# Kernel tuning notes

Measured on AMD Instinct MI355X. Metric: run time of the kernel, lower is better.

Reference implementation:

```python
import jax, jax.numpy as jnp
import numpy as np

B, N, D, H = 1, 4096, 768, 12
HD = D // H
SCALE = HD ** -0.5

def setup_inputs() -> dict:
    key = jax.random.key(0)
    k1, k2, k3 = jax.random.split(key, 3)
    x = jax.random.normal(k1, (B, N, D), dtype=jnp.float32)
    W_qkv = jax.random.normal(k2, (D, 3 * D), dtype=jnp.float32) * (D ** -0.5)
    W_out = jax.random.normal(k3, (D, D), dtype=jnp.float32) * (D ** -0.5)
    b_out = jnp.zeros((D,), dtype=jnp.float32)
    return {"x": x, "W_qkv": W_qkv, "W_out": W_out, "b_out": b_out}

def reference(x, W_qkv, W_out, b_out):
    # qkv projection: (B,N,3D)
    qkv = x @ W_qkv
    q, k, v = jnp.split(qkv, 3, axis=-1)
    # (B,N,D) -> (B,H,N,hd)
    def heads(t):
        return t.reshape(B, N, H, HD).transpose(0, 2, 1, 3)
    q, k, v = heads(q), heads(k), heads(v)
    scores = jnp.einsum('bhnd,bhmd->bhnm', q, k) * SCALE  # (B,H,N,N)
    attn = jax.nn.softmax(scores, axis=-1)
    out = jnp.einsum('bhnm,bhmd->bhnd', attn, v)
    out = out.transpose(0, 2, 1, 3).reshape(B, N, D)
    return out @ W_out + b_out
```

## Files before the change

kernel.cpp:

```cpp
#include <hip/hip_runtime.h>
#include <hip/hip_bf16.h>
#include <math.h>

typedef __attribute__((ext_vector_type(8))) short bf16x8;
typedef __attribute__((ext_vector_type(4))) short bf16x4;
typedef __attribute__((ext_vector_type(4))) float floatx4;
typedef __attribute__((ext_vector_type(4))) unsigned int uint4v;

constexpr int kN  = 4096;
constexpr int kD  = 768;
constexpr int kH  = 12;
constexpr int kHD = 64;
constexpr int k3D = 2304;
constexpr float kQScale = 0.18033688011112042f;

static __device__ __forceinline__ short f2b(float f) {
    __hip_bfloat16 h = __float2bfloat16(f);
    return *reinterpret_cast<short*>(&h);
}

static __device__ __forceinline__ float fast_exp2(float x) {
#if __has_builtin(__builtin_amdgcn_exp2f)
    return __builtin_amdgcn_exp2f(x);
#else
    return exp2f(x);
#endif
}

static __device__ __forceinline__ unsigned cvt_pk_bf16(float lo, float hi) {
    unsigned r;
    asm("v_cvt_pk_bf16_f32 %0, %1, %2" : "=v"(r) : "v"(lo), "v"(hi));
    return r;
}
static __device__ __forceinline__ void permlane32_swap(unsigned &a, unsigned &b) {
    asm("v_permlane32_swap_b32 %0, %1" : "+v"(a), "+v"(b));
}
static __device__ __forceinline__ void permlane16_swap(unsigned &a, unsigned &b) {
    asm("v_permlane16_swap_b32 %0, %1" : "+v"(a), "+v"(b));
}

static __device__ __forceinline__ void async_copy16(const void* g, void* l) {
    __builtin_amdgcn_global_load_lds(
        (const __attribute__((address_space(1))) void*)g,
        (__attribute__((address_space(3))) void*)l, 16, 0, 0);
}

constexpr int kBlkX  = 1536;
constexpr int kBlkWq = 72 * 24;
constexpr int kBlkWo = 24 * 24;

__global__ __launch_bounds__(256)
void prep(const float* __restrict__ x, const float* __restrict__ Wq,
          const float* __restrict__ Wo, short* __restrict__ Xb,
          short* __restrict__ WqT, short* __restrict__ WoT)
{
    const int bid = blockIdx.x;
    const int tid = threadIdx.x;
    if (bid < kBlkX) {
        const int i = bid * 256 + tid;
        const float4* s = reinterpret_cast<const float4*>(x + (size_t)i * 8);
        float4 a = s[0], b = s[1];
        bf16x8 v;
        v[0] = f2b(a.x); v[1] = f2b(a.y); v[2] = f2b(a.z); v[3] = f2b(a.w);
        v[4] = f2b(b.x); v[5] = f2b(b.y); v[6] = f2b(b.z); v[7] = f2b(b.w);
        *reinterpret_cast<bf16x8*>(Xb + (size_t)i * 8) = v;
        return;
    }
    const float* src; short* dst; int R, C, bx, by;
    if (bid < kBlkX + kBlkWq) {
        const int local = bid - kBlkX;
        src = Wq; dst = WqT; R = kD; C = k3D; bx = local % 72; by = local / 72;
    } else {
        const int local = bid - kBlkX - kBlkWq;
        src = Wo; dst = WoT; R = kD; C = kD; bx = local % 24; by = local / 24;
    }
    __shared__ float t[32][33];
    const int c0 = bx * 32, r0 = by * 32;
    const int tx = tid & 31, ty = tid >> 5;
    #pragma unroll
    for (int i = ty; i < 32; i += 8)
        t[i][tx] = src[(size_t)(r0 + i) * C + c0 + tx];
    __syncthreads();
    #pragma unroll
    for (int i = ty; i < 32; i += 8)
        dst[(size_t)(c0 + i) * R + r0 + tx] = f2b(t[tx][i]);
}

template<int MODE>
__device__ __forceinline__
void gemm_core(const short* __restrict__ A, const short* __restrict__ BT,
               const float* __restrict__ bias, float* __restrict__ Cout,
               short* __restrict__ Qh, short* __restrict__ Kh, short* __restrict__ Vt,
               int N, int K)
{
    const int bm   = blockIdx.x * 128;
    const int bn   = blockIdx.y * 128;
    const int tid  = threadIdx.x;
    const int wave = tid >> 6;
    const int lane = tid & 63;
    const int l15  = lane & 15;
    const int quad = lane >> 4;
    const int l3   = l15 & 3;

    __shared__ alignas(16) short As[128 * 32];
    __shared__ alignas(16) short Bs[128 * 32];

    floatx4 acc[4][4] = {};
    const int wm = (wave >> 1) * 64;
    const int wn = (wave & 1) * 64;

    const int srl = lane >> 2;
    const int scc = (lane & 3) ^ (srl & 3);

    for (int k0 = 0; k0 < K; k0 += 32) {
        __syncthreads();
        #pragma unroll
        for (int j = 0; j < 2; ++j) {
            const int rs = 32 * wave + 16 * j;
            async_copy16(&A [(size_t)(bm + rs + srl) * K + k0 + 8 * scc], &As[rs * 32]);
            async_copy16(&BT[(size_t)(bn + rs + srl) * K + k0 + 8 * scc], &Bs[rs * 32]);
        }
        __syncthreads();

        bf16x8 af[4], bfr[4];
        #pragma unroll
        for (int mt = 0; mt < 4; ++mt)
            af[mt] = *reinterpret_cast<const bf16x8*>(&As[(wm + 16 * mt + l15) * 32 + 8 * (quad ^ l3)]);
        #pragma unroll
        for (int nt = 0; nt < 4; ++nt)
            bfr[nt] = *reinterpret_cast<const bf16x8*>(&Bs[(wn + 16 * nt + l15) * 32 + 8 * (quad ^ l3)]);
        #pragma unroll
        for (int mt = 0; mt < 4; ++mt)
            #pragma unroll
            for (int nt = 0; nt < 4; ++nt)
                acc[mt][nt] = __builtin_amdgcn_mfma_f32_16x16x32_bf16(af[mt], bfr[nt], acc[mt][nt], 0, 0, 0);
    }

    #pragma unroll
    for (int mt = 0; mt < 4; ++mt) {
        #pragma unroll
        for (int nt = 0; nt < 4; ++nt) {
            #pragma unroll
            for (int r = 0; r < 4; ++r) {
                const int row = bm + wm + mt * 16 + 4 * quad + r;
                const int col = bn + wn + nt * 16 + l15;
                float v = acc[mt][nt][r];
                if (MODE == 0) {
                    Cout[(size_t)row * N + col] = v + bias[col];
                } else {
                    const int proj   = col / kD;
                    const int within = col - proj * kD;
                    const int h = within >> 6;
                    const int d = within & 63;
                    if (proj == 0)      Qh[((size_t)h * kN + row) * kHD + d] = f2b(v * kQScale);
                    else if (proj == 1) Kh[((size_t)h * kN + row) * kHD + d] = f2b(v);
                    else                Vt[((size_t)h * kHD + d) * kN + row] = f2b(v);
                }
            }
        }
    }
}

__global__ __launch_bounds__(256)
void gemm_qkv(const short* __restrict__ A, const short* __restrict__ BT,
              short* __restrict__ Qh, short* __restrict__ Kh, short* __restrict__ Vt)
{
    gemm_core<1>(A, BT, nullptr, nullptr, Qh, Kh, Vt, k3D, kD);
}

__global__ __launch_bounds__(256)
void gemm_out(const short* __restrict__ A, const short* __restrict__ BT,
              const float* __restrict__ bias, float* __restrict__ Cout)
{
    gemm_core<0>(A, BT, bias, Cout, nullptr, nullptr, nullptr, kD, kD);
}

__global__ __launch_bounds__(256)
void attn(const short* __restrict__ Qh, const short* __restrict__ Kh,
          const short* __restrict__ Vt, short* __restrict__ AO)
{
    const int flat = blockIdx.y * 64 + blockIdx.x;
    const int W    = (flat & 7) * 96 + (flat >> 3);
    const int h    = W >> 6;
    const int q0   = (W & 63) * 64;

    const int tid  = threadIdx.x;
    const int wave = tid >> 6;
    const int lane = tid & 63;
    const int l15  = lane & 15;
    const int quad = lane >> 4;
    const int lx   = l15 & 7;
    const int wm   = wave >> 1;
    const int wk   = wave & 1;

    __shared__ alignas(16) short smem[16384];
    __shared__ float Dr[2][2][16];
    short* Ks0 = smem;
    short* Vs0 = smem + 8192;

    bf16x8 qf[2][2];
    {
        const size_t qb = ((size_t)h * kN + q0 + 32 * wm + l15) * kHD;
        #pragma unroll
        for (int mt = 0; mt < 2; ++mt)
            #pragma unroll
            for (int s = 0; s < 2; ++s)
                qf[mt][s] = *reinterpret_cast<const bf16x8*>(
                    &Qh[qb + (size_t)(16 * mt) * kHD + 32 * s + 8 * quad]);
    }

    bf16x8 onesf;
    #pragma unroll
    for (int i = 0; i < 8; ++i) onesf[i] = (short)0x3F80;

    floatx4 oacc[2][4] = {};
    floatx4 dacc[2] = {};

    const int srl = lane >> 3;
    const int scc = (lane & 7) ^ srl;

    const size_t kbase = (size_t)h * kN * kHD;
    const size_t vbase = (size_t)h * kHD * kN;

    auto stage = [&](int b, int kv0) {
        #pragma unroll
        for (int j = 0; j < 2; ++j) {
            const int r0 = 16 * wave + 8 * j;
            async_copy16(&Kh[kbase + (size_t)(kv0 + r0 + srl) * kHD + 8 * scc],
                         Ks0 + b * 4096 + r0 * 64);
            async_copy16(&Vt[vbase + (size_t)(r0 + srl) * kN + kv0 + 8 * scc],
                         Vs0 + b * 4096 + r0 * 64);
        }
    };

    constexpr int kNT = kN / 64;
    int cur = 0;
    stage(0, 0);

    for (int t = 0; t < kNT; ++t) {
        __syncthreads();
        if (t + 1 < kNT) stage(cur ^ 1, (t + 1) * 64);

        const short* Kc = Ks0 + cur * 4096;
        const short* Vc = Vs0 + cur * 4096;

        floatx4 sacc[2][2] = {};
        __builtin_amdgcn_s_setprio(1);
        #pragma unroll
        for (int nt = 0; nt < 2; ++nt) {
            #pragma unroll
            for (int s = 0; s < 2; ++s) {
                bf16x8 kf = *reinterpret_cast<const bf16x8*>(
                    &Kc[(32 * wk + 16 * nt + l15) * 64 + 8 * ((4 * s + quad) ^ lx)]);
                #pragma unroll
                for (int mt = 0; mt < 2; ++mt)
                    sacc[mt][nt] = __builtin_amdgcn_mfma_f32_16x16x32_bf16(
                        kf, qf[mt][s], sacc[mt][nt], 0, 0, 0);
            }
        }
        __builtin_amdgcn_s_setprio(0);

        bf16x8 pa[2];
        #pragma unroll
        for (int mt = 0; mt < 2; ++mt) {
            float e[2][4];
            #pragma unroll
            for (int nt = 0; nt < 2; ++nt)
                #pragma unroll
                for (int r = 0; r < 4; ++r)
                    e[nt][r] = fast_exp2(sacc[mt][nt][r]);
            unsigned x0 = cvt_pk_bf16(e[0][0], e[0][1]);
            unsigned y0 = cvt_pk_bf16(e[1][0], e[1][1]);
            unsigned x1 = cvt_pk_bf16(e[0][2], e[0][3]);
            unsigned y1 = cvt_pk_bf16(e[1][2], e[1][3]);
            permlane32_swap(x0, y0);
            permlane16_swap(x0, y0);
            permlane32_swap(x1, y1);
            permlane16_swap(x1, y1);
            union { uint4v u; bf16x8 v; } pu;
            pu.u[0] = x0; pu.u[1] = x1; pu.u[2] = y0; pu.u[3] = y1;
            pa[mt] = pu.v;
        }

        __builtin_amdgcn_s_setprio(1);
        #pragma unroll
        for (int dt = 0; dt < 4; ++dt) {
            bf16x8 vv = *reinterpret_cast<const bf16x8*>(
                &Vc[(16 * dt + l15) * 64 + 8 * ((4 * wk + quad) ^ lx)]);
            #pragma unroll
            for (int mt = 0; mt < 2; ++mt)
                oacc[mt][dt] = __builtin_amdgcn_mfma_f32_16x16x32_bf16(
                    pa[mt], vv, oacc[mt][dt], 0, 0, 0);
        }
        #pragma unroll
        for (int mt = 0; mt < 2; ++mt)
            dacc[mt] = __builtin_amdgcn_mfma_f32_16x16x32_bf16(
                pa[mt], onesf, dacc[mt], 0, 0, 0);
        __builtin_amdgcn_s_setprio(0);

        cur ^= 1;
    }

    __syncthreads();
    float* red = reinterpret_cast<float*>(smem);
    if (wk == 1) {
        #pragma unroll
        for (int mt = 0; mt < 2; ++mt)
            #pragma unroll
            for (int dt = 0; dt < 4; ++dt)
                *reinterpret_cast<floatx4*>(
                    &red[wm * 2048 + (mt * 4 + dt) * 256 + l15 * 16 + quad * 4]) =
                    oacc[mt][dt];
        if (l15 == 0) {
            #pragma unroll
            for (int mt = 0; mt < 2; ++mt)
                #pragma unroll
                for (int r = 0; r < 4; ++r)
                    Dr[wm][mt][4 * quad + r] = dacc[mt][r];
        }
    }
    __syncthreads();
    if (wk == 0) {
        #pragma unroll
        for (int mt = 0; mt < 2; ++mt) {
            #pragma unroll
            for (int dt = 0; dt < 4; ++dt)
                oacc[mt][dt] += *reinterpret_cast<const floatx4*>(
                    &red[wm * 2048 + (mt * 4 + dt) * 256 + l15 * 16 + quad * 4]);
            float inv[4];
            #pragma unroll
            for (int r = 0; r < 4; ++r)
                inv[r] = 1.0f / (dacc[mt][r] + Dr[wm][mt][4 * quad + r]);
            #pragma unroll
            for (int dt = 0; dt < 4; ++dt) {
                #pragma unroll
                for (int r = 0; r < 4; ++r) {
                    const int row = q0 + 32 * wm + 16 * mt + 4 * quad + r;
                    const int col = h * kHD + 16 * dt + l15;
                    AO[(size_t)row * kD + col] = f2b(oacc[mt][dt][r] * inv[r]);
                }
            }
        }
    }
}

extern "C" void kernel_launch(void* const* d_in, const int* in_sizes, int n_in,
                              void* d_out, int out_size, void* d_ws, size_t ws_size,
                              hipStream_t stream)
{
    const float* x     = (const float*)d_in[0];
    const float* W_qkv = (const float*)d_in[1];
    const float* W_out = (const float*)d_in[2];
    const float* b_out = (const float*)d_in[3];
    float* out = (float*)d_out;

    const size_t HNHD = (size_t)kH * kN * kHD;
    short* Qh    = (short*)d_ws;
    short* Kh    = Qh + HNHD;
    short* Vt    = Kh + HNHD;
    short* Xb    = Vt + HNHD;
    short* WqkvT = Xb + (size_t)kN * kD;
    short* WoutT = WqkvT + (size_t)k3D * kD;
    short* AO    = Xb;
    (void)in_sizes; (void)n_in; (void)out_size; (void)ws_size;

    prep<<<dim3(kBlkX + kBlkWq + kBlkWo), dim3(256), 0, stream>>>(
        x, W_qkv, W_out, Xb, WqkvT, WoutT);

    gemm_qkv<<<dim3(kN / 128, k3D / 128), dim3(256), 0, stream>>>(
        Xb, WqkvT, Qh, Kh, Vt);
    attn<<<dim3(kN / 64, kH), dim3(256), 0, stream>>>(Qh, Kh, Vt, AO);
    gemm_out<<<dim3(kN / 128, kD / 128), dim3(256), 0, stream>>>(
        AO, WoutT, b_out, out);
}
```

Measured before the change: 212.3 us.

## Software-pipeline QK/exp of next tile with PV of current tile

Restructures the attention KV loop so the QK^T plus exp2 for tile t+1 is issued before the PV matmul of tile t completes, using two ping-pong probability register sets and a manually unrolled-by-two loop. Global and LDS staging pointers are also precomputed outside the loop to cut per-iteration address arithmetic. The aim is to overlap the exp and cross-lane permute work with MFMA work and hide latency, at the cost of higher register pressure from the extra P buffers.

```diff
diff --git a/kernel.cpp b/kernel.cpp
--- a/kernel.cpp
+++ b/kernel.cpp
@@ -219,31 +219,22 @@
     const int srl = lane >> 3;
     const int scc = (lane & 7) ^ srl;
 
-    const size_t kbase = (size_t)h * kN * kHD;
-    const size_t vbase = (size_t)h * kHD * kN;
+    const short* kgp = &Kh[(size_t)h * kN * kHD +
+                           (size_t)(16 * wave + srl) * kHD + 8 * scc];
+    const short* vgp = &Vt[(size_t)h * kHD * kN +
+                           (size_t)(16 * wave + srl) * kN + 8 * scc];
+    short* kls = Ks0 + (16 * wave) * 64;
+    short* vls = Vs0 + (16 * wave) * 64;
 
     auto stage = [&](int b, int kv0) {
         #pragma unroll
         for (int j = 0; j < 2; ++j) {
-            const int r0 = 16 * wave + 8 * j;
-            async_copy16(&Kh[kbase + (size_t)(kv0 + r0 + srl) * kHD + 8 * scc],
-                         Ks0 + b * 4096 + r0 * 64);
-            async_copy16(&Vt[vbase + (size_t)(r0 + srl) * kN + kv0 + 8 * scc],
-                         Vs0 + b * 4096 + r0 * 64);
+            async_copy16(kgp + (size_t)(kv0 + 8 * j) * kHD, kls + b * 4096 + (8 * j) * 64);
+            async_copy16(vgp + (size_t)(8 * j) * kN + kv0,  vls + b * 4096 + (8 * j) * 64);
         }
     };
 
-    constexpr int kNT = kN / 64;
-    int cur = 0;
-    stage(0, 0);
-
-    for (int t = 0; t < kNT; ++t) {
-        __syncthreads();
-        if (t + 1 < kNT) stage(cur ^ 1, (t + 1) * 64);
-
-        const short* Kc = Ks0 + cur * 4096;
-        const short* Vc = Vs0 + cur * 4096;
-
+    auto qk_exp = [&](const short* Kc, bf16x8 (&pa)[2]) {
         floatx4 sacc[2][2] = {};
         __builtin_amdgcn_s_setprio(1);
         #pragma unroll
@@ -259,8 +250,6 @@
             }
         }
         __builtin_amdgcn_s_setprio(0);
-
-        bf16x8 pa[2];
         #pragma unroll
         for (int mt = 0; mt < 2; ++mt) {
             float e[2][4];
@@ -281,7 +270,9 @@
             pu.u[0] = x0; pu.u[1] = x1; pu.u[2] = y0; pu.u[3] = y1;
             pa[mt] = pu.v;
         }
-
+    };
+
+    auto pv = [&](const short* Vc, const bf16x8 (&pa)[2]) {
         __builtin_amdgcn_s_setprio(1);
         #pragma unroll
         for (int dt = 0; dt < 4; ++dt) {
@@ -297,9 +288,35 @@
             dacc[mt] = __builtin_amdgcn_mfma_f32_16x16x32_bf16(
                 pa[mt], onesf, dacc[mt], 0, 0, 0);
         __builtin_amdgcn_s_setprio(0);
-
+    };
+
+    constexpr int kNT = kN / 64;
+    bf16x8 paA[2], paB[2];
+
+    stage(0, 0);
+    __syncthreads();
+    stage(1, 64);
+    qk_exp(Ks0, paA);
+    int cur = 1;
+
+    for (int tp = 0; tp < 31; ++tp) {
+        const int u = 2 * tp + 1;
+        pv(Vs0 + (cur ^ 1) * 4096, paA);
+        __syncthreads();
+        stage(cur ^ 1, (u + 1) * 64);
+        qk_exp(Ks0 + cur * 4096, paB);
         cur ^= 1;
-    }
+        pv(Vs0 + (cur ^ 1) * 4096, paB);
+        __syncthreads();
+        stage(cur ^ 1, (u + 2) * 64);
+        qk_exp(Ks0 + cur * 4096, paA);
+        cur ^= 1;
+    }
+
+    pv(Vs0 + (cur ^ 1) * 4096, paA);
+    __syncthreads();
+    qk_exp(Ks0 + cur * 4096, paB);
+    pv(Vs0 + cur * 4096, paB);
 
     __syncthreads();
     float* red = reinterpret_cast<float*>(smem);
```

Result: faster. 197.0 us (-7.2%).

## Load K/V fragments directly from global into registers, dropping LDS staging

Applied to the files above, without the earlier changes.

Replaces the double-buffered async LDS staging of K and V tiles, along with the per-tile __syncthreads, with direct per-wave global loads of the MFMA fragments into registers. The next tile is prefetched in registers right after it is consumed. This removes barrier and LDS traffic, but the two waves sharing each wk half (wm=0/1) now fetch identical K/V data from global/L2, and the scattered 16-byte fragment loads are less coalesced. Load latency is hidden only by the single-step register prefetch.

```diff
diff --git a/kernel.cpp b/kernel.cpp
--- a/kernel.cpp
+++ b/kernel.cpp
@@ -189,14 +189,11 @@
     const int lane = tid & 63;
     const int l15  = lane & 15;
     const int quad = lane >> 4;
-    const int lx   = l15 & 7;
     const int wm   = wave >> 1;
     const int wk   = wave & 1;
 
-    __shared__ alignas(16) short smem[16384];
+    __shared__ alignas(16) float red[4096];
     __shared__ float Dr[2][2][16];
-    short* Ks0 = smem;
-    short* Vs0 = smem + 8192;
 
     bf16x8 qf[2][2];
     {
@@ -216,51 +213,40 @@
     floatx4 oacc[2][4] = {};
     floatx4 dacc[2] = {};
 
-    const int srl = lane >> 3;
-    const int scc = (lane & 7) ^ srl;
-
-    const size_t kbase = (size_t)h * kN * kHD;
-    const size_t vbase = (size_t)h * kHD * kN;
-
-    auto stage = [&](int b, int kv0) {
-        #pragma unroll
-        for (int j = 0; j < 2; ++j) {
-            const int r0 = 16 * wave + 8 * j;
-            async_copy16(&Kh[kbase + (size_t)(kv0 + r0 + srl) * kHD + 8 * scc],
-                         Ks0 + b * 4096 + r0 * 64);
-            async_copy16(&Vt[vbase + (size_t)(r0 + srl) * kN + kv0 + 8 * scc],
-                         Vs0 + b * 4096 + r0 * 64);
-        }
-    };
-
-    constexpr int kNT = kN / 64;
-    int cur = 0;
-    stage(0, 0);
-
-    for (int t = 0; t < kNT; ++t) {
-        __syncthreads();
-        if (t + 1 < kNT) stage(cur ^ 1, (t + 1) * 64);
-
-        const short* Kc = Ks0 + cur * 4096;
-        const short* Vc = Vs0 + cur * 4096;
-
-        floatx4 sacc[2][2] = {};
+    const short* kp = Kh + (size_t)h * kN * kHD
+                         + (size_t)(32 * wk + l15) * kHD + 8 * quad;
+    const short* vp = Vt + (size_t)h * kHD * kN
+                         + (size_t)l15 * kN + 32 * wk + 8 * quad;
+
+    auto load_k = [&](int kv0, bf16x8 (&kf)[2][2]) {
+        #pragma unroll
+        for (int nt = 0; nt < 2; ++nt)
+            #pragma unroll
+            for (int s = 0; s < 2; ++s)
+                kf[nt][s] = *reinterpret_cast<const bf16x8*>(
+                    kp + (size_t)(kv0 + 16 * nt) * kHD + 32 * s);
+    };
+    auto load_v = [&](int kv0, bf16x8 (&vv)[4]) {
+        #pragma unroll
+        for (int dt = 0; dt < 4; ++dt)
+            vv[dt] = *reinterpret_cast<const bf16x8*>(
+                vp + (size_t)(16 * dt) * kN + kv0);
+    };
+
+    auto qk = [&](const bf16x8 (&kf)[2][2], floatx4 (&sacc)[2][2]) {
         __builtin_amdgcn_s_setprio(1);
         #pragma unroll
-        for (int nt = 0; nt < 2; ++nt) {
-            #pragma unroll
-            for (int s = 0; s < 2; ++s) {
-                bf16x8 kf = *reinterpret_cast<const bf16x8*>(
-                    &Kc[(32 * wk + 16 * nt + l15) * 64 + 8 * ((4 * s + quad) ^ lx)]);
+        for (int nt = 0; nt < 2; ++nt)
+            #pragma unroll
+            for (int s = 0; s < 2; ++s)
                 #pragma unroll
                 for (int mt = 0; mt < 2; ++mt)
                     sacc[mt][nt] = __builtin_amdgcn_mfma_f32_16x16x32_bf16(
-                        kf, qf[mt][s], sacc[mt][nt], 0, 0, 0);
-            }
-        }
+                        kf[nt][s], qf[mt][s], sacc[mt][nt], 0, 0, 0);
         __builtin_amdgcn_s_setprio(0);
-
-        bf16x8 pa[2];
+    };
+
+    auto expack = [&](const floatx4 (&sacc)[2][2], bf16x8 (&pa)[2]) {
         #pragma unroll
         for (int mt = 0; mt < 2; ++mt) {
             float e[2][4];
@@ -281,28 +267,37 @@
             pu.u[0] = x0; pu.u[1] = x1; pu.u[2] = y0; pu.u[3] = y1;
             pa[mt] = pu.v;
         }
-
+    };
+
+    auto pv = [&](const bf16x8 (&vv)[4], const bf16x8 (&pa)[2]) {
         __builtin_amdgcn_s_setprio(1);
         #pragma unroll
-        for (int dt = 0; dt < 4; ++dt) {
-            bf16x8 vv = *reinterpret_cast<const bf16x8*>(
-                &Vc[(16 * dt + l15) * 64 + 8 * ((4 * wk + quad) ^ lx)]);
+        for (int dt = 0; dt < 4; ++dt)
             #pragma unroll
             for (int mt = 0; mt < 2; ++mt)
                 oacc[mt][dt] = __builtin_amdgcn_mfma_f32_16x16x32_bf16(
-                    pa[mt], vv, oacc[mt][dt], 0, 0, 0);
-        }
+                    pa[mt], vv[dt], oacc[mt][dt], 0, 0, 0);
         #pragma unroll
         for (int mt = 0; mt < 2; ++mt)
             dacc[mt] = __builtin_amdgcn_mfma_f32_16x16x32_bf16(
                 pa[mt], onesf, dacc[mt], 0, 0, 0);
         __builtin_amdgcn_s_setprio(0);
-
-        cur ^= 1;
-    }
-
-    __syncthreads();
-    float* red = reinterpret_cast<float*>(smem);
+    };
+
+    constexpr int kNT = kN / 64;
+    bf16x8 kf[2][2], vv[4], pa[2];
+    load_k(0, kf);
+    load_v(0, vv);
+
+    for (int u = 0; u < kNT; ++u) {
+        floatx4 sacc[2][2] = {};
+        qk(kf, sacc);
+        if (u + 1 < kNT) load_k((u + 1) * 64, kf);
+        expack(sacc, pa);
+        pv(vv, pa);
+        if (u + 1 < kNT) load_v((u + 1) * 64, vv);
+    }
+
     if (wk == 1) {
         #pragma unroll
         for (int mt = 0; mt < 2; ++mt)
```

After: 295.1 us. 39.0% more time.
